# Optimization experiments

Measured on AMD Instinct MI355X. Metric: run time of the kernel, lower is better.

Reference implementation:

```python
import jax, jax.numpy as jnp
import numpy as np

N_HEAD = 16
HEAD_DIM = 64  # n_embd // n_head = 1024 // 16


def setup_inputs() -> dict:
    key = jax.random.key(0)
    k1, k2, k3 = jax.random.split(key, 3)
    B, T, C = 4, 2048, 1024
    x = jax.random.normal(k1, (B, T, C), dtype=jnp.float32)
    # torch Linear weight is (out, in); we store transposed (in, out) for x @ W
    w_qkv = jax.random.normal(k2, (C, 3 * C), dtype=jnp.float32) * (1.0 / np.sqrt(C))
    w_out = jax.random.normal(k3, (C, C), dtype=jnp.float32) * (1.0 / np.sqrt(C))
    return {"x": x, "w_qkv": w_qkv, "w_out": w_out}


def reference(x, w_qkv, w_out):
    B, T, C = x.shape
    scale = 1.0 / np.sqrt(HEAD_DIM).astype(np.float32)
    qkv = x @ w_qkv                                   # [B, T, 3C]
    q, k, v = jnp.split(qkv, 3, axis=2)
    def heads(t):  # [B, T, C] -> [B, H, T, Dh]
        return t.reshape(B, T, N_HEAD, HEAD_DIM).transpose(0, 2, 1, 3)
    q, k, v = heads(q), heads(k), heads(v)
    att = jnp.einsum('bhqd,bhkd->bhqk', q, k) * scale  # [B, H, T, T]
    causal = jnp.tril(jnp.ones((T, T), dtype=bool))
    att = jnp.where(causal[None, None], att, jnp.float32(-jnp.inf))
    att = jax.nn.softmax(att, axis=-1)
    y = jnp.einsum('bhqk,bhkd->bhqd', att, v)          # [B, H, T, Dh]
    y = y.transpose(0, 2, 1, 3).reshape(B, T, C)
    return y @ w_out
```

## Files before the change

kernel.cpp:

```cpp
#include <hip/hip_runtime.h>
#include <hip/hip_bf16.h>

#define B_ 4
#define T_ 2048
#define C_ 1024
#define H_ 16
#define D_ 64

typedef __bf16 bf16x8 __attribute__((ext_vector_type(8)));
typedef float f32x4 __attribute__((ext_vector_type(4)));
typedef float f32x16 __attribute__((ext_vector_type(16)));

__device__ __forceinline__ unsigned short f2bs(float f) {
    __hip_bfloat16 h = __float2bfloat16(f);
    return *reinterpret_cast<unsigned short*>(&h);
}

__device__ __forceinline__ unsigned cvtpk(float a, float b) {
    unsigned r;
    asm("v_cvt_pk_bf16_f32 %0, %1, %2" : "=v"(r) : "v"(a), "v"(b));
    return r;
}

__device__ __forceinline__ void plane32swap(unsigned& a, unsigned& b, int hi) {
#if __has_builtin(__builtin_amdgcn_permlane32_swap)
    typedef int i32x2 __attribute__((ext_vector_type(2)));
    i32x2 r = __builtin_amdgcn_permlane32_swap((int)a, (int)b, false, false);
    a = (unsigned)r.x; b = (unsigned)r.y;
#else
    unsigned v = hi ? a : b;
    unsigned e = __shfl_xor(v, 32);
    unsigned na = hi ? e : a;
    unsigned nb = hi ? b : e;
    a = na; b = nb;
#endif
}

__device__ __forceinline__ int swz(int row, int col) {
    return (row * 64 + col) ^ ((row & 7) << 3);
}

__device__ __forceinline__ void gload16(const void* g, void* l) {
    auto gp = (const __attribute__((address_space(1))) void*)(g);
    auto lp = (__attribute__((address_space(3))) void*)(uintptr_t)(l);
    __builtin_amdgcn_global_load_lds(gp, lp, 16, 0, 0);
}

__global__ __launch_bounds__(256)
void cvt_f32_to_bf16(const float* __restrict__ in, unsigned short* __restrict__ out, int n4) {
    int i = blockIdx.x * 256 + threadIdx.x;
    if (i >= n4) return;
    float4 v = ((const float4*)in)[i];
    union { unsigned short h[4]; uint2 u; } pk;
    pk.h[0] = f2bs(v.x); pk.h[1] = f2bs(v.y);
    pk.h[2] = f2bs(v.z); pk.h[3] = f2bs(v.w);
    ((uint2*)out)[i] = pk.u;
}

__global__ __launch_bounds__(256)
void transpose_weights(const float* __restrict__ in1, unsigned short* __restrict__ out1,
                       const float* __restrict__ in2, unsigned short* __restrict__ out2) {
    __shared__ float tile[64][65];
    const int tx = threadIdx.x & 63;
    const int ty = threadIdx.x >> 6;
    const bool second = blockIdx.x >= 48;
    const float* in = second ? in2 : in1;
    unsigned short* out = second ? out2 : out1;
    const int C = second ? 1024 : 3072;
    const int R = 1024;
    const int c0 = (second ? (blockIdx.x - 48) : blockIdx.x) * 64;
    const int r0 = blockIdx.y * 64;
    #pragma unroll
    for (int i = 0; i < 16; ++i) {
        int r = ty * 16 + i;
        tile[r][tx] = in[(size_t)(r0 + r) * C + c0 + tx];
    }
    __syncthreads();
    #pragma unroll
    for (int i = 0; i < 16; ++i) {
        int r = ty * 16 + i;
        out[(size_t)(c0 + r) * R + r0 + tx] = f2bs(tile[tx][r]);
    }
}

template<int MODE>
__global__ __launch_bounds__(256)
void gemm_bt(const unsigned short* __restrict__ A,
             const unsigned short* __restrict__ Bt,
             float* __restrict__ Out, int N_out,
             unsigned short* __restrict__ Qb,
             unsigned short* __restrict__ Kb,
             unsigned short* __restrict__ Vt,
             int K) {
    __shared__ alignas(16) unsigned short As[2][128 * 64];
    __shared__ alignas(16) unsigned short Bs[2][128 * 64];
    const int tid = threadIdx.x;
    const int l = tid & 63;
    const int c16 = l & 15, lq = l >> 4;
    const int wv = tid >> 6;
    const int wrow = wv >> 1, wcol = wv & 1;
    const int m0 = blockIdx.x * 128, n0 = blockIdx.y * 128;

    f32x4 acc[4][4];
    #pragma unroll
    for (int i = 0; i < 4; ++i)
        #pragma unroll
        for (int j = 0; j < 4; ++j)
            acc[i][j] = f32x4{0.f, 0.f, 0.f, 0.f};

    const int srow = tid >> 3;
    const int scs  = tid & 7;
    const int ldsbase = (tid & ~63) * 8;

    auto stage = [&](int k0, int buf) {
        #pragma unroll
        for (int p = 0; p < 4; ++p) {
            int row = p * 32 + srow;
            int csw = 8 * (scs ^ (row & 7));
            gload16(&A[(size_t)(m0 + row) * K + k0 + csw], &As[buf][p * 2048 + ldsbase]);
            gload16(&Bt[(size_t)(n0 + row) * K + k0 + csw], &Bs[buf][p * 2048 + ldsbase]);
        }
    };

    stage(0, 0);
    const int NK = K >> 6;
    for (int i = 0; i < NK; ++i) {
        __syncthreads();
        if (i + 1 < NK) stage((i + 1) << 6, (i + 1) & 1);
        const unsigned short* Al = As[i & 1];
        const unsigned short* Bl = Bs[i & 1];
        #pragma unroll
        for (int kk = 0; kk < 64; kk += 32) {
            bf16x8 af[4], bfv[4];
            int koff = kk + lq * 8;
            #pragma unroll
            for (int t = 0; t < 4; ++t) {
                af[t]  = *(const bf16x8*)&Al[swz(wrow * 64 + t * 16 + c16, koff)];
                bfv[t] = *(const bf16x8*)&Bl[swz(wcol * 64 + t * 16 + c16, koff)];
            }
            #pragma unroll
            for (int mi = 0; mi < 4; ++mi)
                #pragma unroll
                for (int ni = 0; ni < 4; ++ni)
                    acc[mi][ni] = __builtin_amdgcn_mfma_f32_16x16x32_bf16(
                        af[mi], bfv[ni], acc[mi][ni], 0, 0, 0);
        }
    }

    #pragma unroll
    for (int mi = 0; mi < 4; ++mi) {
        #pragma unroll
        for (int ni = 0; ni < 4; ++ni) {
            #pragma unroll
            for (int r = 0; r < 4; ++r) {
                float v = acc[mi][ni][r];
                int row = m0 + wrow * 64 + mi * 16 + lq * 4 + r;
                int col = n0 + wcol * 64 + ni * 16 + c16;
                if (MODE == 1) {
                    Out[(size_t)row * N_out + col] = v;
                } else {
                    int which = col >> 10;
                    int c = col & 1023;
                    int h = c >> 6, d = c & 63;
                    int b = row >> 11, t = row & 2047;
                    int bh = b * H_ + h;
                    if (which == 0)
                        Qb[((size_t)(bh * T_ + t)) * D_ + d] = f2bs(v * 0.1803368801111204f);
                    else if (which == 1)
                        Kb[((size_t)(bh * T_ + t)) * D_ + d] = f2bs(v);
                    else
                        Vt[((size_t)(bh * D_ + d)) * T_ + t] = f2bs(v);
                }
            }
        }
    }
}

__global__ __launch_bounds__(256, 2)
void attn_fwd(const unsigned short* __restrict__ Qb,
              const unsigned short* __restrict__ Kb,
              const unsigned short* __restrict__ Vt,
              unsigned short* __restrict__ Y) {
    __shared__ alignas(16) unsigned short Ks[2][64 * 64];
    __shared__ alignas(16) unsigned short Vs[2][64 * 64];
    const int tid = threadIdx.x;
    const int wv = tid >> 6;
    const int l = tid & 63;
    const int r32 = l & 31;
    const int hi = l >> 5;
    const int hi8 = hi * 8;
    const int bh = blockIdx.x & 63;
    const int qp = blockIdx.x >> 6;
    const unsigned short* Kp = Kb + (size_t)bh * T_ * D_;
    const unsigned short* Vp = Vt + (size_t)bh * D_ * T_;
    const unsigned short* Qbase = Qb + (size_t)bh * T_ * D_;
    const int b = bh >> 4, h = bh & 15;
    const int srow = tid >> 3;
    const int scs  = tid & 7;
    const int scol_sw = 8 * (scs ^ (srow & 7));
    const int wbase = wv * 512;

    #pragma unroll
    for (int half = 0; half < 2; ++half) {
        const int qc = (half == 0) ? qp : 15 - qp;
        const int q0w = qc * 128 + wv * 32;
        const int nt = 2 * qc + 2;
        const int qg = q0w + r32;

        bf16x8 qf[4];
        #pragma unroll
        for (int ds = 0; ds < 4; ++ds)
            qf[ds] = *(const bf16x8*)&Qbase[(size_t)qg * 64 + ds * 16 + hi8];

        f32x16 o[2];
        #pragma unroll
        for (int e = 0; e < 16; ++e) { o[0][e] = 0.f; o[1][e] = 0.f; }
        float lsum = 0.f;

        __syncthreads();
        gload16(&Kp[(size_t)srow * 64 + scol_sw],        &Ks[0][wbase]);
        gload16(&Kp[(size_t)(srow + 32) * 64 + scol_sw], &Ks[0][2048 + wbase]);
        gload16(&Vp[(size_t)srow * T_ + scol_sw],        &Vs[0][wbase]);
        gload16(&Vp[(size_t)(srow + 32) * T_ + scol_sw], &Vs[0][2048 + wbase]);

        for (int it = 0; it < nt; ++it) {
            const int kb = it * 64;
            __syncthreads();
            if (it + 1 < nt) {
                const int kn = kb + 64;
                unsigned short* Kd = Ks[(it + 1) & 1];
                unsigned short* Vd = Vs[(it + 1) & 1];
                gload16(&Kp[(size_t)(kn + srow) * 64 + scol_sw],        &Kd[wbase]);
                gload16(&Kp[(size_t)(kn + srow + 32) * 64 + scol_sw],   &Kd[2048 + wbase]);
                gload16(&Vp[(size_t)srow * T_ + kn + scol_sw],          &Vd[wbase]);
                gload16(&Vp[(size_t)(srow + 32) * T_ + kn + scol_sw],   &Vd[2048 + wbase]);
            }
            if (kb > q0w + 31) continue;
            const unsigned short* Kl = Ks[it & 1];
            const unsigned short* Vl = Vs[it & 1];

            f32x16 s[2];
            #pragma unroll
            for (int e = 0; e < 16; ++e) { s[0][e] = 0.f; s[1][e] = 0.f; }
            __builtin_amdgcn_s_setprio(1);
            #pragma unroll
            for (int kt = 0; kt < 2; ++kt)
                #pragma unroll
                for (int ds = 0; ds < 4; ++ds) {
                    bf16x8 af = *(const bf16x8*)&Kl[swz(32 * kt + r32, ds * 16 + hi8)];
                    s[kt] = __builtin_amdgcn_mfma_f32_32x32x16_bf16(af, qf[ds], s[kt], 0, 0, 0);
                }
            __builtin_amdgcn_s_setprio(0);
            if (kb + 63 > q0w) {
                #pragma unroll
                for (int kt = 0; kt < 2; ++kt)
                    #pragma unroll
                    for (int m = 0; m < 4; ++m)
                        #pragma unroll
                        for (int r = 0; r < 4; ++r)
                            if (kb + 32 * kt + 8 * m + r + 4 * hi > qg)
                                s[kt][4 * m + r] = -1e30f;
            }
            float rs = 0.f;
            #pragma unroll
            for (int kt = 0; kt < 2; ++kt)
                #pragma unroll
                for (int e = 0; e < 16; ++e) {
                    float p = exp2f(s[kt][e]);
                    s[kt][e] = p;
                    rs += p;
                }
            lsum += rs;
            bf16x8 pb[4];
            #pragma unroll
            for (int ks = 0; ks < 4; ++ks) {
                const int kt = ks >> 1;
                const int m0 = (ks & 1) * 2;
                unsigned a0 = cvtpk(s[kt][4 * m0 + 0], s[kt][4 * m0 + 1]);
                unsigned a1 = cvtpk(s[kt][4 * m0 + 2], s[kt][4 * m0 + 3]);
                unsigned b0 = cvtpk(s[kt][4 * m0 + 4], s[kt][4 * m0 + 5]);
                unsigned b1 = cvtpk(s[kt][4 * m0 + 6], s[kt][4 * m0 + 7]);
                plane32swap(a0, b0, hi);
                plane32swap(a1, b1, hi);
                uint4 u = {a0, a1, b0, b1};
                pb[ks] = *reinterpret_cast<bf16x8*>(&u);
            }
            __builtin_amdgcn_s_setprio(1);
            #pragma unroll
            for (int dt = 0; dt < 2; ++dt)
                #pragma unroll
                for (int ks = 0; ks < 4; ++ks) {
                    bf16x8 va = *(const bf16x8*)&Vl[swz(32 * dt + r32, ks * 16 + hi8)];
                    o[dt] = __builtin_amdgcn_mfma_f32_32x32x16_bf16(va, pb[ks], o[dt], 0, 0, 0);
                }
            __builtin_amdgcn_s_setprio(0);
        }

        float lt = lsum + __shfl_xor(lsum, 32);
        float inv = 1.f / lt;
        #pragma unroll
        for (int dt = 0; dt < 2; ++dt)
            #pragma unroll
            for (int m = 0; m < 4; ++m) {
                uint2 w;
                w.x = cvtpk(o[dt][4 * m + 0] * inv, o[dt][4 * m + 1] * inv);
                w.y = cvtpk(o[dt][4 * m + 2] * inv, o[dt][4 * m + 3] * inv);
                int d = 32 * dt + 8 * m + 4 * hi;
                *(uint2*)&Y[((size_t)(b * T_ + qg)) * C_ + h * D_ + d] = w;
            }
    }
}

extern "C" void kernel_launch(void* const* d_in, const int* in_sizes, int n_in,
                              void* d_out, int out_size, void* d_ws, size_t ws_size,
                              hipStream_t stream) {
    const float* x     = (const float*)d_in[0];
    const float* w_qkv = (const float*)d_in[1];
    const float* w_out = (const float*)d_in[2];
    float* out = (float*)d_out;
    char* ws = (char*)d_ws;

    unsigned short* xb  = (unsigned short*)(ws);
    unsigned short* wqt = (unsigned short*)(ws + (16u << 20));
    unsigned short* wot = (unsigned short*)(ws + (22u << 20));
    unsigned short* Qb  = (unsigned short*)(ws + (24u << 20));
    unsigned short* Kb  = (unsigned short*)(ws + (40u << 20));
    unsigned short* Vt  = (unsigned short*)(ws + (56u << 20));
    unsigned short* Yb  = (unsigned short*)(ws + (72u << 20));

    cvt_f32_to_bf16<<<8192, 256, 0, stream>>>(x, xb, (B_ * T_ * C_) / 4);
    transpose_weights<<<dim3(64, 16), 256, 0, stream>>>(w_qkv, wqt, w_out, wot);
    gemm_bt<0><<<dim3(64, 24), 256, 0, stream>>>(xb, wqt, nullptr, 3072, Qb, Kb, Vt, 1024);
    attn_fwd<<<512, 256, 0, stream>>>(Qb, Kb, Vt, Yb);
    gemm_bt<1><<<dim3(64, 8), 256, 0, stream>>>(Yb, wot, out, 1024, nullptr, nullptr, nullptr, 1024);
}
```

Before: 171.2 us.

## Replace QKV projection GEMM with 256x256-tile, 8-wave pipelined kernel

Adds a new GEMM kernel with 256x256 output tiles, 512 threads and 128 KB of double-buffered LDS. It interleaves staggered global-to-LDS loads with four MFMA phases per K-step, using explicit barriers and s_setprio. It replaces the 128x128 QKV projection GEMM to raise data reuse per tile and overlap loads with compute. The grid shrinks to 384 blocks, which risks poor CU coverage and limits occupancy through LDS and register pressure.

```diff
diff --git a/kernel.cpp b/kernel.cpp
--- a/kernel.cpp
+++ b/kernel.cpp
@@ -45,6 +45,10 @@
     auto lp = (__attribute__((address_space(3))) void*)(uintptr_t)(l);
     __builtin_amdgcn_global_load_lds(gp, lp, 16, 0, 0);
 }
+
+#define FULLBAR() do { __builtin_amdgcn_sched_barrier(0); \
+                       __builtin_amdgcn_s_barrier(); \
+                       __builtin_amdgcn_sched_barrier(0); } while (0)
 
 __global__ __launch_bounds__(256)
 void cvt_f32_to_bf16(const float* __restrict__ in, unsigned short* __restrict__ out, int n4) {
@@ -80,6 +84,167 @@
     for (int i = 0; i < 16; ++i) {
         int r = ty * 16 + i;
         out[(size_t)(c0 + r) * R + r0 + tx] = f2bs(tile[tx][r]);
+    }
+}
+
+template<int MODE, int K>
+__global__ __launch_bounds__(512, 2)
+void gemm256(const unsigned short* __restrict__ A,
+             const unsigned short* __restrict__ Bt,
+             float* __restrict__ Out, int N_out,
+             unsigned short* __restrict__ Qb,
+             unsigned short* __restrict__ Kb,
+             unsigned short* __restrict__ Vt) {
+    __shared__ alignas(16) unsigned short L[2][4][128 * 64];
+    const int tid = threadIdx.x;
+    const int l = tid & 63;
+    const int c16 = l & 15, lq = l >> 4;
+    const int wv = tid >> 6;
+    const int wm = wv >> 2;
+    const int wn = wv & 3;
+    const int m0 = blockIdx.x * 256, n0 = blockIdx.y * 256;
+    constexpr int NT = K / 64;
+
+    f32x4 acc[8][4];
+    #pragma unroll
+    for (int i = 0; i < 8; ++i)
+        #pragma unroll
+        for (int j = 0; j < 4; ++j)
+            acc[i][j] = f32x4{0.f, 0.f, 0.f, 0.f};
+
+    const int srow = tid >> 3;
+    const int scs  = tid & 7;
+    const int ldsbase = (tid & ~63) * 8;
+
+    auto stage = [&](const unsigned short* M, int row0, int k0, unsigned short* dst) {
+        #pragma unroll
+        for (int r = 0; r < 2; ++r) {
+            int row = r * 64 + srow;
+            int csw = 8 * (scs ^ (row & 7));
+            gload16(&M[(size_t)(row0 + row) * K + k0 + csw], &dst[r * 4096 + ldsbase]);
+        }
+    };
+
+    stage(A,  m0,       0, L[0][0]);
+    stage(A,  m0 + 128, 0, L[0][1]);
+    stage(Bt, n0,       0, L[0][2]);
+    stage(Bt, n0 + 128, 0, L[0][3]);
+    if (NT > 1) stage(A, m0, 64, L[1][0]);
+
+    bf16x8 af[4][2], bf[2][2], bg[2][2];
+    const int brow0 = (wn & 1) * 64;
+
+    for (int t = 0; t < NT; ++t) {
+        const unsigned short* ap = L[t & 1][wm];
+        const unsigned short* bp = L[t & 1][2 + (wn >> 1)];
+        const int kn = (t + 1) * 64;
+
+        if (t == NT - 1) asm volatile("s_waitcnt vmcnt(0)" ::: "memory");
+        else             asm volatile("s_waitcnt vmcnt(2)" ::: "memory");
+        __builtin_amdgcn_sched_barrier(0);
+        #pragma unroll
+        for (int mi = 0; mi < 4; ++mi)
+            #pragma unroll
+            for (int kk = 0; kk < 2; ++kk)
+                af[mi][kk] = *(const bf16x8*)&ap[swz(mi * 16 + c16, kk * 32 + lq * 8)];
+        #pragma unroll
+        for (int ni = 0; ni < 2; ++ni)
+            #pragma unroll
+            for (int kk = 0; kk < 2; ++kk)
+                bf[ni][kk] = *(const bf16x8*)&bp[swz(brow0 + ni * 16 + c16, kk * 32 + lq * 8)];
+        if (t + 1 < NT) stage(A, m0 + 128, kn, L[(t + 1) & 1][1]);
+        FULLBAR();
+        __builtin_amdgcn_s_setprio(1);
+        #pragma unroll
+        for (int mi = 0; mi < 4; ++mi)
+            #pragma unroll
+            for (int ni = 0; ni < 2; ++ni)
+                #pragma unroll
+                for (int kk = 0; kk < 2; ++kk)
+                    acc[mi][ni] = __builtin_amdgcn_mfma_f32_16x16x32_bf16(
+                        af[mi][kk], bf[ni][kk], acc[mi][ni], 0, 0, 0);
+        __builtin_amdgcn_s_setprio(0);
+        FULLBAR();
+
+        #pragma unroll
+        for (int ni = 0; ni < 2; ++ni)
+            #pragma unroll
+            for (int kk = 0; kk < 2; ++kk)
+                bg[ni][kk] = *(const bf16x8*)&bp[swz(brow0 + (ni + 2) * 16 + c16, kk * 32 + lq * 8)];
+        if (t + 1 < NT) stage(Bt, n0, kn, L[(t + 1) & 1][2]);
+        FULLBAR();
+        __builtin_amdgcn_s_setprio(1);
+        #pragma unroll
+        for (int mi = 0; mi < 4; ++mi)
+            #pragma unroll
+            for (int ni = 0; ni < 2; ++ni)
+                #pragma unroll
+                for (int kk = 0; kk < 2; ++kk)
+                    acc[mi][ni + 2] = __builtin_amdgcn_mfma_f32_16x16x32_bf16(
+                        af[mi][kk], bg[ni][kk], acc[mi][ni + 2], 0, 0, 0);
+        __builtin_amdgcn_s_setprio(0);
+        FULLBAR();
+
+        #pragma unroll
+        for (int mi = 0; mi < 4; ++mi)
+            #pragma unroll
+            for (int kk = 0; kk < 2; ++kk)
+                af[mi][kk] = *(const bf16x8*)&ap[swz((mi + 4) * 16 + c16, kk * 32 + lq * 8)];
+        if (t + 1 < NT) stage(Bt, n0 + 128, kn, L[(t + 1) & 1][3]);
+        FULLBAR();
+        __builtin_amdgcn_s_setprio(1);
+        #pragma unroll
+        for (int mi = 0; mi < 4; ++mi)
+            #pragma unroll
+            for (int ni = 0; ni < 2; ++ni)
+                #pragma unroll
+                for (int kk = 0; kk < 2; ++kk)
+                    acc[mi + 4][ni + 2] = __builtin_amdgcn_mfma_f32_16x16x32_bf16(
+                        af[mi][kk], bg[ni][kk], acc[mi + 4][ni + 2], 0, 0, 0);
+        __builtin_amdgcn_s_setprio(0);
+        FULLBAR();
+
+        if (t + 2 < NT) stage(A, m0, (t + 2) * 64, L[t & 1][0]);
+        FULLBAR();
+        __builtin_amdgcn_s_setprio(1);
+        #pragma unroll
+        for (int mi = 0; mi < 4; ++mi)
+            #pragma unroll
+            for (int ni = 0; ni < 2; ++ni)
+                #pragma unroll
+                for (int kk = 0; kk < 2; ++kk)
+                    acc[mi + 4][ni] = __builtin_amdgcn_mfma_f32_16x16x32_bf16(
+                        af[mi][kk], bf[ni][kk], acc[mi + 4][ni], 0, 0, 0);
+        __builtin_amdgcn_s_setprio(0);
+        FULLBAR();
+    }
+
+    #pragma unroll
+    for (int mi = 0; mi < 8; ++mi) {
+        #pragma unroll
+        for (int ni = 0; ni < 4; ++ni) {
+            #pragma unroll
+            for (int r = 0; r < 4; ++r) {
+                float v = acc[mi][ni][r];
+                int row = m0 + wm * 128 + mi * 16 + lq * 4 + r;
+                int col = n0 + wn * 64 + ni * 16 + c16;
+                if (MODE == 1) {
+                    Out[(size_t)row * N_out + col] = v;
+                } else {
+                    int which = col >> 10;
+                    int c = col & 1023;
+                    int h = c >> 6, d = c & 63;
+                    int b = row >> 11, t = row & 2047;
+                    int bh = b * H_ + h;
+                    if (which == 0)
+                        Qb[((size_t)(bh * T_ + t)) * D_ + d] = f2bs(v * 0.1803368801111204f);
+                    else if (which == 1)
+                        Kb[((size_t)(bh * T_ + t)) * D_ + d] = f2bs(v);
+                    else
+                        Vt[((size_t)(bh * D_ + d)) * T_ + t] = f2bs(v);
+                }
+            }
+        }
     }
 }
 
@@ -330,7 +495,7 @@
 
     cvt_f32_to_bf16<<<8192, 256, 0, stream>>>(x, xb, (B_ * T_ * C_) / 4);
     transpose_weights<<<dim3(64, 16), 256, 0, stream>>>(w_qkv, wqt, w_out, wot);
-    gemm_bt<0><<<dim3(64, 24), 256, 0, stream>>>(xb, wqt, nullptr, 3072, Qb, Kb, Vt, 1024);
+    gemm256<0, 1024><<<dim3(32, 12), 512, 0, stream>>>(xb, wqt, nullptr, 3072, Qb, Kb, Vt);
     attn_fwd<<<512, 256, 0, stream>>>(Qb, Kb, Vt, Yb);
     gemm_bt<1><<<dim3(64, 8), 256, 0, stream>>>(Yb, wot, out, 1024, nullptr, nullptr, nullptr, 1024);
 }
```

Result: slower. 192.2 us (+12.3%).
